# Kernel tuning notes

Hardware: AMD Instinct MI355X
Metric: run time of the kernel (lower is better)

The kernel has to match this reference:

```python
import jax, jax.numpy as jnp
import numpy as np

B, T, IN, OUT, H = 4096, 512, 16, 16, 64


def setup_inputs() -> dict:
    key = jax.random.key(0)
    ks = jax.random.split(key, 9)
    s = jnp.float32(0.1)  # keep gates in a sane range
    return {
        "X": jax.random.normal(ks[0], (B, T, IN), jnp.float32),
        "enc_Wih": jax.random.normal(ks[1], (4 * H, IN), jnp.float32) * s,
        "enc_Whh": jax.random.normal(ks[2], (4 * H, H), jnp.float32) * s,
        "enc_b": jax.random.normal(ks[3], (4 * H,), jnp.float32) * s,
        "dec_Wih": jax.random.normal(ks[4], (4 * H, OUT), jnp.float32) * s,
        "dec_Whh": jax.random.normal(ks[5], (4 * H, H), jnp.float32) * s,
        "dec_b": jax.random.normal(ks[6], (4 * H,), jnp.float32) * s,
        "head_W": jax.random.normal(ks[7], (OUT, H), jnp.float32) * s,
        "head_b": jax.random.normal(ks[8], (OUT,), jnp.float32) * s,
    }


def _cell(h, c, gates):
    # torch LSTM gate order: input, forget, cell(g), output
    i, f, g, o = jnp.split(gates, 4, axis=-1)
    c = jax.nn.sigmoid(f) * c + jax.nn.sigmoid(i) * jnp.tanh(g)
    h = jax.nn.sigmoid(o) * jnpp_tanh(c) if False else jax.nn.sigmoid(o) * jnp.tanh(c)
    return h, c


def reference(X, enc_Wih, enc_Whh, enc_b, dec_Wih, dec_Whh, dec_b, head_W, head_b):
    Bv, Tv, _ = X.shape
    Hh = enc_Whh.shape[1]

    # ---- encoder: single-layer LSTM, keep only final (h, c) ----
    # precompute input projections for all timesteps: (T, B, 4H)
    Xp = jnp.swapaxes(jnp.einsum('bti,gi->btg', X, enc_Wih) + enc_b, 0, 1)

    def enc_step(carry, xp):
        h, c = carry
        gates = xp + h @ enc_Whh.T  # (B, 4H)
        h, c = _cell(h, c, gates)
        return (h, c), None

    z = jnp.zeros((Bv, Hh), X.dtype)
    (h, c), _ = jax.lax.scan(enc_step, (z, z), Xp)

    prev0 = jnp.zeros((Bv, head_W.shape[0]), X.dtype)  # BOS = zeros

    def dec_step(carry, _):
        h, c, prev = carry
        gates = prev @ dec_Wih.T + h @ dec_Whh.T + dec_b
        h, c = _cell(h, c, gates)
        pred = h @ head_W.T + head_b  # (B, OUT)
        return (h, c, pred), pred

    _, preds = jax.lax.scan(dec_step, (h, c, prev0), None, length=Tv)
    return jnp.swapaxes(preds, 0, 1)  # (B, T, OUT)
```

## Files before the change

kernel.cpp:

```cpp
#include <hip/hip_runtime.h>
#include <hip/hip_bf16.h>

#define TPB 256
#define TSTEPS 512

typedef __attribute__((ext_vector_type(8))) short bfrag;
typedef __attribute__((ext_vector_type(4))) float f32x4;

#define LD4(p) (*reinterpret_cast<const float4*>(p))
#define MFMA(a, b, c) __builtin_amdgcn_mfma_f32_16x16x32_bf16((a), (b), (c), 0, 0, 0)

__device__ __forceinline__ float fast_rcp(float x) {
  float r; asm("v_rcp_f32 %0, %1" : "=v"(r) : "v"(x)); return r;
}
__device__ __forceinline__ float sigf(float x) { return fast_rcp(1.f + __expf(-x)); }
__device__ __forceinline__ float tanh_f(float x) {
  float y = fminf(fmaxf(x, -15.f), 15.f);
  float e = __expf(2.f * y);
  return (e - 1.f) * fast_rcp(e + 1.f);
}
__device__ __forceinline__ unsigned short f2bf(float f) {
  __hip_bfloat16 h = __float2bfloat16(f);
  return *reinterpret_cast<unsigned short*>(&h);
}
__device__ __forceinline__ float bf2f(unsigned short u) {
  __hip_bfloat16 h; *reinterpret_cast<unsigned short*>(&h) = u;
  return __bfloat162float(h);
}

#define SPLIT8(V, FH, FL) do { \
  _Pragma("unroll") \
  for (int j_ = 0; j_ < 8; ++j_) { \
    const unsigned short h_ = f2bf(V[j_]); \
    FH[j_] = (short)h_; \
    FL[j_] = (short)f2bf(V[j_] - bf2f(h_)); \
  } } while (0)

#define HBI(buf, hl, b) ((((buf)*2 + (hl))*16 + (b)) * 72)

__global__ void __launch_bounds__(TPB, 1) lstm_mfma(
    const float* __restrict__ X,    const float* __restrict__ eWih,
    const float* __restrict__ eWhh, const float* __restrict__ eb,
    const float* __restrict__ dWih, const float* __restrict__ dWhh,
    const float* __restrict__ db,   const float* __restrict__ hWp,
    const float* __restrict__ hbp,  float* __restrict__ out)
{
  __shared__ __align__(16) unsigned long long XF[4096];
  __shared__ __align__(16) unsigned short HB[2*2*16*72];
  __shared__ __align__(16) float HWs[16*72];
  __shared__ float HBS[16];

  const int tid = threadIdx.x;
  const int w = tid >> 6, l = tid & 63;
  const int c = l & 15, q = l >> 4;
  const int bb0 = blockIdx.x * 16;

  for (int i = tid; i < 4096; i += TPB) XF[i] = 0ULL;
  for (int i = tid; i < 2*2*16*72; i += TPB) HB[i] = 0;
  {
    const int o = tid >> 4, k4 = tid & 15;
    *reinterpret_cast<float4*>(&HWs[o*72 + k4*4]) = LD4(hWp + o*64 + k4*4);
    if (tid < 16) HBS[tid] = hbp[tid];
  }

  bfrag wh_h[4][2], wh_l[4][2], wi_h[4], wi_l[4];
  float bias[4];
  #pragma unroll
  for (int G = 0; G < 4; ++G) {
    const int g = G*64 + w*16 + c;
    bias[G] = eb[g];
    #pragma unroll
    for (int kt = 0; kt < 2; ++kt) {
      float v[8];
      #pragma unroll
      for (int j = 0; j < 8; ++j) v[j] = eWhh[g*64 + kt*32 + q*8 + j];
      SPLIT8(v, wh_h[G][kt], wh_l[G][kt]);
    }
    {
      float v[8];
      #pragma unroll
      for (int j = 0; j < 8; ++j) { const int k = q*8 + j; v[j] = (k < 16) ? eWih[g*16 + k] : 0.f; }
      SPLIT8(v, wi_h[G], wi_l[G]);
    }
  }
  bfrag hwf_h[2], hwf_l[2];
  #pragma unroll
  for (int kt = 0; kt < 2; ++kt) {
    float v[8];
    #pragma unroll
    for (int j = 0; j < 8; ++j) v[j] = hWp[c*64 + kt*32 + q*8 + j];
    SPLIT8(v, hwf_h[kt], hwf_l[kt]);
  }
  const float hbv = hbp[c];

  float cc[4] = {0.f, 0.f, 0.f, 0.f};

  for (int t = 0; t < TSTEPS; ++t) {
    const int tt = t & 15;
    if (tt == 0) {
      __syncthreads();
      #pragma unroll
      for (int r = 0; r < 4; ++r) {
        const int fidx = r * TPB + tid;
        const int i4 = fidx & 3, ts = (fidx >> 2) & 15, b = fidx >> 6;
        const float4 v = LD4(X + ((size_t)(bb0 + b) * TSTEPS + (t + ts)) * 16 + i4 * 4);
        const unsigned short hx = f2bf(v.x), hy = f2bf(v.y), hz = f2bf(v.z), hw2 = f2bf(v.w);
        const unsigned short lx = f2bf(v.x - bf2f(hx)), ly = f2bf(v.y - bf2f(hy)),
                             lz = f2bf(v.z - bf2f(hz)), lw = f2bf(v.w - bf2f(hw2));
        const int dp = i4 & 1, slot = (i4 >> 1) * 16 + b;
        XF[((ts*2 + dp)*2 + 0)*64 + slot] =
            (unsigned long long)((unsigned)hx | ((unsigned)hy << 16)) |
            ((unsigned long long)((unsigned)hz | ((unsigned)hw2 << 16)) << 32);
        XF[((ts*2 + dp)*2 + 1)*64 + slot] =
            (unsigned long long)((unsigned)lx | ((unsigned)ly << 16)) |
            ((unsigned long long)((unsigned)lz | ((unsigned)lw << 16)) << 32);
      }
    }
    __syncthreads();
    const int rb = t & 1;

    bfrag ah_h[2], ah_l[2], ax_h, ax_l;
    #pragma unroll
    for (int kt = 0; kt < 2; ++kt) {
      ah_h[kt] = *reinterpret_cast<const bfrag*>(&HB[HBI(rb, 0, c) + kt*32 + q*8]);
      ah_l[kt] = *reinterpret_cast<const bfrag*>(&HB[HBI(rb, 1, c) + kt*32 + q*8]);
    }
    {
      union { bfrag f; unsigned long long d2[2]; } uh, ul;
      uh.d2[0] = XF[((tt*2 + 0)*2 + 0)*64 + l]; uh.d2[1] = XF[((tt*2 + 1)*2 + 0)*64 + l];
      ul.d2[0] = XF[((tt*2 + 0)*2 + 1)*64 + l]; ul.d2[1] = XF[((tt*2 + 1)*2 + 1)*64 + l];
      ax_h = uh.f; ax_l = ul.f;
    }

    f32x4 acc[4];
    #pragma unroll
    for (int G = 0; G < 4; ++G) { f32x4 z = {bias[G], bias[G], bias[G], bias[G]}; acc[G] = z; }
    #pragma unroll
    for (int G = 0; G < 4; ++G) {
      acc[G] = MFMA(ax_h, wi_h[G], acc[G]);
      acc[G] = MFMA(ax_h, wi_l[G], acc[G]);
      acc[G] = MFMA(ax_l, wi_h[G], acc[G]);
      #pragma unroll
      for (int kt = 0; kt < 2; ++kt) {
        acc[G] = MFMA(ah_h[kt], wh_h[G][kt], acc[G]);
        acc[G] = MFMA(ah_h[kt], wh_l[G][kt], acc[G]);
        acc[G] = MFMA(ah_l[kt], wh_h[G][kt], acc[G]);
      }
    }

    const int wb = rb ^ 1;
    #pragma unroll
    for (int r = 0; r < 4; ++r) {
      const float ig = sigf(acc[0][r]), fg = sigf(acc[1][r]);
      const float gg = tanh_f(acc[2][r]), og = sigf(acc[3][r]);
      cc[r] = fg * cc[r] + ig * gg;
      const float h = og * tanh_f(cc[r]);
      const unsigned short hh = f2bf(h);
      const unsigned short hl2 = f2bf(h - bf2f(hh));
      const int b = q*4 + r;
      HB[HBI(wb, 0, b) + w*16 + c] = hh;
      HB[HBI(wb, 1, b) + w*16 + c] = hl2;
    }
  }

  #pragma unroll
  for (int G = 0; G < 4; ++G) {
    const int g = G*64 + w*16 + c;
    bias[G] = db[g];
    #pragma unroll
    for (int kt = 0; kt < 2; ++kt) {
      float v[8];
      #pragma unroll
      for (int j = 0; j < 8; ++j) v[j] = dWhh[g*64 + kt*32 + q*8 + j];
      SPLIT8(v, wh_h[G][kt], wh_l[G][kt]);
    }
  }

  for (int t = 0; t < TSTEPS; ++t) {
    __syncthreads();
    const int rb = t & 1;
    bfrag ah_h[2], ah_l[2];
    #pragma unroll
    for (int kt = 0; kt < 2; ++kt) {
      ah_h[kt] = *reinterpret_cast<const bfrag*>(&HB[HBI(rb, 0, c) + kt*32 + q*8]);
      ah_l[kt] = *reinterpret_cast<const bfrag*>(&HB[HBI(rb, 1, c) + kt*32 + q*8]);
    }
    if (w == 3 && t > 0) {
      f32x4 hd = {hbv, hbv, hbv, hbv};
      #pragma unroll
      for (int kt = 0; kt < 2; ++kt) {
        hd = MFMA(ah_h[kt], hwf_h[kt], hd);
        hd = MFMA(ah_h[kt], hwf_l[kt], hd);
        hd = MFMA(ah_l[kt], hwf_h[kt], hd);
      }
      #pragma unroll
      for (int r = 0; r < 4; ++r)
        out[((size_t)(bb0 + q*4 + r) * TSTEPS + (t - 1)) * 16 + c] = hd[r];
    }

    f32x4 acc[4];
    #pragma unroll
    for (int G = 0; G < 4; ++G) { f32x4 z = {bias[G], bias[G], bias[G], bias[G]}; acc[G] = z; }
    #pragma unroll
    for (int G = 0; G < 4; ++G) {
      #pragma unroll
      for (int kt = 0; kt < 2; ++kt) {
        acc[G] = MFMA(ah_h[kt], wh_h[G][kt], acc[G]);
        acc[G] = MFMA(ah_h[kt], wh_l[G][kt], acc[G]);
        acc[G] = MFMA(ah_l[kt], wh_h[G][kt], acc[G]);
      }
    }

    const int wb = rb ^ 1;
    #pragma unroll
    for (int r = 0; r < 4; ++r) {
      const float ig = sigf(acc[0][r]), fg = sigf(acc[1][r]);
      const float gg = tanh_f(acc[2][r]), og = sigf(acc[3][r]);
      cc[r] = fg * cc[r] + ig * gg;
      const float h = og * tanh_f(cc[r]);
      const unsigned short hh = f2bf(h);
      const unsigned short hl2 = f2bf(h - bf2f(hh));
      const int b = q*4 + r;
      HB[HBI(wb, 0, b) + w*16 + c] = hh;
      HB[HBI(wb, 1, b) + w*16 + c] = hl2;
    }

    if (t == 0) {
      #pragma unroll
      for (int G = 0; G < 4; ++G) {
        const int g = G*64 + w*16 + c;
        float dwv[16];
        #pragma unroll
        for (int o4 = 0; o4 < 4; ++o4) {
          const float4 v = LD4(dWih + g*16 + o4*4);
          dwv[o4*4+0] = v.x; dwv[o4*4+1] = v.y; dwv[o4*4+2] = v.z; dwv[o4*4+3] = v.w;
        }
        float bb = db[g];
        #pragma unroll
        for (int o = 0; o < 16; ++o) bb += dwv[o] * HBS[o];
        bias[G] = bb;
        #pragma unroll
        for (int kt = 0; kt < 2; ++kt) {
          float v[8];
          #pragma unroll
          for (int j = 0; j < 8; ++j) {
            const int k = kt*32 + q*8 + j;
            float ww = dWhh[g*64 + k];
            #pragma unroll
            for (int o = 0; o < 16; ++o) ww += dwv[o] * HWs[o*72 + k];
            v[j] = ww;
          }
          SPLIT8(v, wh_h[G][kt], wh_l[G][kt]);
        }
      }
    }
  }

  __syncthreads();
  if (w == 3) {
    const int rb = TSTEPS & 1;
    bfrag ah_h[2], ah_l[2];
    #pragma unroll
    for (int kt = 0; kt < 2; ++kt) {
      ah_h[kt] = *reinterpret_cast<const bfrag*>(&HB[HBI(rb, 0, c) + kt*32 + q*8]);
      ah_l[kt] = *reinterpret_cast<const bfrag*>(&HB[HBI(rb, 1, c) + kt*32 + q*8]);
    }
    f32x4 hd = {hbv, hbv, hbv, hbv};
    #pragma unroll
    for (int kt = 0; kt < 2; ++kt) {
      hd = MFMA(ah_h[kt], hwf_h[kt], hd);
      hd = MFMA(ah_h[kt], hwf_l[kt], hd);
      hd = MFMA(ah_l[kt], hwf_h[kt], hd);
    }
    #pragma unroll
    for (int r = 0; r < 4; ++r)
      out[((size_t)(bb0 + q*4 + r) * TSTEPS + (TSTEPS - 1)) * 16 + c] = hd[r];
  }
}

extern "C" void kernel_launch(void* const* d_in, const int* in_sizes, int n_in,
                              void* d_out, int out_size, void* d_ws, size_t ws_size,
                              hipStream_t stream) {
  (void)in_sizes; (void)n_in; (void)d_ws; (void)ws_size; (void)out_size;
  const float* X    = (const float*)d_in[0];
  const float* eWih = (const float*)d_in[1];
  const float* eWhh = (const float*)d_in[2];
  const float* eb   = (const float*)d_in[3];
  const float* dWih = (const float*)d_in[4];
  const float* dWhh = (const float*)d_in[5];
  const float* db   = (const float*)d_in[6];
  const float* hW   = (const float*)d_in[7];
  const float* hb   = (const float*)d_in[8];
  float* out = (float*)d_out;

  lstm_mfma<<<dim3(256), dim3(TPB), 0, stream>>>(
      X, eWih, eWhh, eb, dWih, dWhh, db, hW, hb, out);
}
```

Measured before the change: 1.112 ms.

## Halve batch rows per block to double grid size and allow two blocks per CU

Each block now handles 8 batch rows instead of 16, so 512 blocks launch instead of 256 and launch bounds allow two blocks per CU. This is meant to fill more of the device's CUs and to hide the latency of the serial recurrence by running more independent blocks at once. The MFMA tiles still compute 16 rows, so half of each tile is wasted work; lanes with q>=2 skip the cell update, the h stores and the output writes. The hi/lo bf16 split also switches to truncating the high part, which saves a conversion.

```diff
diff --git a/kernel.cpp b/kernel.cpp
--- a/kernel.cpp
+++ b/kernel.cpp
@@ -3,6 +3,7 @@
 
 #define TPB 256
 #define TSTEPS 512
+#define NROWS 8
 
 typedef __attribute__((ext_vector_type(8))) short bfrag;
 typedef __attribute__((ext_vector_type(4))) float f32x4;
@@ -26,6 +27,11 @@
 __device__ __forceinline__ float bf2f(unsigned short u) {
   __hip_bfloat16 h; *reinterpret_cast<unsigned short*>(&h) = u;
   return __bfloat162float(h);
+}
+__device__ __forceinline__ void split_tr(float x, unsigned short& hi, unsigned short& lo) {
+  const unsigned u = __float_as_uint(x) & 0xffff0000u;
+  hi = (unsigned short)(u >> 16);
+  lo = f2bf(x - __uint_as_float(u));
 }
 
 #define SPLIT8(V, FH, FL) do { \
@@ -38,7 +44,7 @@
 
 #define HBI(buf, hl, b) ((((buf)*2 + (hl))*16 + (b)) * 72)
 
-__global__ void __launch_bounds__(TPB, 1) lstm_mfma(
+__global__ void __launch_bounds__(TPB, 2) lstm_mfma(
     const float* __restrict__ X,    const float* __restrict__ eWih,
     const float* __restrict__ eWhh, const float* __restrict__ eb,
     const float* __restrict__ dWih, const float* __restrict__ dWhh,
@@ -53,7 +59,7 @@
   const int tid = threadIdx.x;
   const int w = tid >> 6, l = tid & 63;
   const int c = l & 15, q = l >> 4;
-  const int bb0 = blockIdx.x * 16;
+  const int bb0 = blockIdx.x * NROWS;
 
   for (int i = tid; i < 4096; i += TPB) XF[i] = 0ULL;
   for (int i = tid; i < 2*2*16*72; i += TPB) HB[i] = 0;
@@ -100,13 +106,13 @@
     if (tt == 0) {
       __syncthreads();
       #pragma unroll
-      for (int r = 0; r < 4; ++r) {
+      for (int r = 0; r < 2; ++r) {
         const int fidx = r * TPB + tid;
         const int i4 = fidx & 3, ts = (fidx >> 2) & 15, b = fidx >> 6;
         const float4 v = LD4(X + ((size_t)(bb0 + b) * TSTEPS + (t + ts)) * 16 + i4 * 4);
-        const unsigned short hx = f2bf(v.x), hy = f2bf(v.y), hz = f2bf(v.z), hw2 = f2bf(v.w);
-        const unsigned short lx = f2bf(v.x - bf2f(hx)), ly = f2bf(v.y - bf2f(hy)),
-                             lz = f2bf(v.z - bf2f(hz)), lw = f2bf(v.w - bf2f(hw2));
+        unsigned short hx, lx, hy, ly, hz, lz, hw2, lw;
+        split_tr(v.x, hx, lx); split_tr(v.y, hy, ly);
+        split_tr(v.z, hz, lz); split_tr(v.w, hw2, lw);
         const int dp = i4 & 1, slot = (i4 >> 1) * 16 + b;
         XF[((ts*2 + dp)*2 + 0)*64 + slot] =
             (unsigned long long)((unsigned)hx | ((unsigned)hy << 16)) |
@@ -149,17 +155,19 @@
     }
 
     const int wb = rb ^ 1;
-    #pragma unroll
-    for (int r = 0; r < 4; ++r) {
-      const float ig = sigf(acc[0][r]), fg = sigf(acc[1][r]);
-      const float gg = tanh_f(acc[2][r]), og = sigf(acc[3][r]);
-      cc[r] = fg * cc[r] + ig * gg;
-      const float h = og * tanh_f(cc[r]);
-      const unsigned short hh = f2bf(h);
-      const unsigned short hl2 = f2bf(h - bf2f(hh));
-      const int b = q*4 + r;
-      HB[HBI(wb, 0, b) + w*16 + c] = hh;
-      HB[HBI(wb, 1, b) + w*16 + c] = hl2;
+    if (q < 2) {
+      #pragma unroll
+      for (int r = 0; r < 4; ++r) {
+        const float ig = sigf(acc[0][r]), fg = sigf(acc[1][r]);
+        const float gg = tanh_f(acc[2][r]), og = sigf(acc[3][r]);
+        cc[r] = fg * cc[r] + ig * gg;
+        const float h = og * tanh_f(cc[r]);
+        unsigned short hh, hl2;
+        split_tr(h, hh, hl2);
+        const int b = q*4 + r;
+        HB[HBI(wb, 0, b) + w*16 + c] = hh;
+        HB[HBI(wb, 1, b) + w*16 + c] = hl2;
+      }
     }
   }
 
@@ -193,9 +201,11 @@
         hd = MFMA(ah_h[kt], hwf_l[kt], hd);
         hd = MFMA(ah_l[kt], hwf_h[kt], hd);
       }
-      #pragma unroll
-      for (int r = 0; r < 4; ++r)
-        out[((size_t)(bb0 + q*4 + r) * TSTEPS + (t - 1)) * 16 + c] = hd[r];
+      if (q < 2) {
+        #pragma unroll
+        for (int r = 0; r < 4; ++r)
+          out[((size_t)(bb0 + q*4 + r) * TSTEPS + (t - 1)) * 16 + c] = hd[r];
+      }
     }
 
     f32x4 acc[4];
@@ -212,17 +222,19 @@
     }
 
     const int wb = rb ^ 1;
-    #pragma unroll
-    for (int r = 0; r < 4; ++r) {
-      const float ig = sigf(acc[0][r]), fg = sigf(acc[1][r]);
-      const float gg = tanh_f(acc[2][r]), og = sigf(acc[3][r]);
-      cc[r] = fg * cc[r] + ig * gg;
-      const float h = og * tanh_f(cc[r]);
-      const unsigned short hh = f2bf(h);
-      const unsigned short hl2 = f2bf(h - bf2f(hh));
-      const int b = q*4 + r;
-      HB[HBI(wb, 0, b) + w*16 + c] = hh;
-      HB[HBI(wb, 1, b) + w*16 + c] = hl2;
+    if (q < 2) {
+      #pragma unroll
+      for (int r = 0; r < 4; ++r) {
+        const float ig = sigf(acc[0][r]), fg = sigf(acc[1][r]);
+        const float gg = tanh_f(acc[2][r]), og = sigf(acc[3][r]);
+        cc[r] = fg * cc[r] + ig * gg;
+        const float h = og * tanh_f(cc[r]);
+        unsigned short hh, hl2;
+        split_tr(h, hh, hl2);
+        const int b = q*4 + r;
+        HB[HBI(wb, 0, b) + w*16 + c] = hh;
+        HB[HBI(wb, 1, b) + w*16 + c] = hl2;
+      }
     }
 
     if (t == 0) {
@@ -272,9 +284,11 @@
       hd = MFMA(ah_h[kt], hwf_l[kt], hd);
       hd = MFMA(ah_l[kt], hwf_h[kt], hd);
     }
-    #pragma unroll
-    for (int r = 0; r < 4; ++r)
-      out[((size_t)(bb0 + q*4 + r) * TSTEPS + (TSTEPS - 1)) * 16 + c] = hd[r];
+    if (q < 2) {
+      #pragma unroll
+      for (int r = 0; r < 4; ++r)
+        out[((size_t)(bb0 + q*4 + r) * TSTEPS + (TSTEPS - 1)) * 16 + c] = hd[r];
+    }
   }
 }
 
@@ -293,6 +307,6 @@
   const float* hb   = (const float*)d_in[8];
   float* out = (float*)d_out;
 
-  lstm_mfma<<<dim3(256), dim3(TPB), 0, stream>>>(
+  lstm_mfma<<<dim3(4096 / NROWS), dim3(TPB), 0, stream>>>(
       X, eWih, eWhh, eb, dWih, dWhh, db, hW, hb, out);
 }
```

New measurement: 1.800 ms. +61.8%, slower.
